# Performance work log

Measured on AMD Instinct MI355X. Metric: run time of the kernel, lower is better.

## Reference

```python
import jax, jax.numpy as jnp
import numpy as np

B, S, D = 4, 1024, 2048
NH, NKV, HD = 16, 8, 128
N_EXP, TOP_K, RANK, ALPHA = 4, 2, 16, 32
LORA_SCALE = ALPHA / RANK
EPS = 1e-6
NEG_INF = -1e9


def setup_inputs() -> dict:
    key = jax.random.key(0)
    ks = jax.random.split(key, 12)
    inv_freq = 1.0 / (10000.0 ** (jnp.arange(0, HD, 2, dtype=jnp.float32) / HD))
    pos = jnp.arange(S, dtype=jnp.float32)
    freqs = pos[:, None] * inv_freq[None, :]            # [S, HD/2]
    emb = jnp.concatenate([freqs, freqs], axis=-1)      # [S, HD]
    cos = jnp.broadcast_to(jnp.cos(emb)[None], (B, S, HD))
    sin = jnp.broadcast_to(jnp.sin(emb)[None], (B, S, HD))
    s = 0.02
    return {
        "hidden_states": jax.random.normal(ks[0], (B, S, D), jnp.float32),
        "cos": cos,
        "sin": sin,
        "Wq": jax.random.normal(ks[1], (NH * HD, D), jnp.float32) * s,
        "Wk": jax.random.normal(ks[2], (NKV * HD, D), jnp.float32) * s,
        "Wv": jax.random.normal(ks[3], (NKV * HD, D), jnp.float32) * s,
        "Wo": jax.random.normal(ks[4], (D, NH * HD), jnp.float32) * s,
        "q_norm_w": jnp.ones((HD,), jnp.float32),
        "k_norm_w": jnp.ones((HD,), jnp.float32),
        "gate_w": jax.random.normal(ks[5], (N_EXP, D), jnp.float32) * s,
        "loraA": jax.random.normal(ks[6], (N_EXP, RANK, NH * HD), jnp.float32) * s,
        "loraB": jax.random.normal(ks[7], (N_EXP, D, RANK), jnp.float32) * s,
    }


def _rms_norm(x, w):
    # per-head-dim RMSNorm (Qwen3 style), computed in fp32
    var = jnp.mean(jnp.square(x.astype(jnp.float32)), axis=-1, keepdims=True)
    return (x.astype(jnp.float32) * jax.lax.rsqrt(var + EPS)).astype(x.dtype) * w


def _rotate_half(x):
    x1, x2 = jnp.split(x, 2, axis=-1)
    return jnp.concatenate([-x2, x1], axis=-1)


def reference(hidden_states, cos, sin, Wq, Wk, Wv, Wo, q_norm_w, k_norm_w, gate_w, loraA, loraB):
    b, s, d = hidden_states.shape
    scaling = HD ** -0.5

    # ---- router (top-k of softmax over 4 experts) ----
    flat = hidden_states.reshape(-1, d)                       # [T, D]
    router_logits = flat @ gate_w.T                           # [T, E]
    probs = jax.nn.softmax(router_logits.astype(jnp.float32), axis=-1)
    top_w, top_idx = jax.lax.top_k(probs, TOP_K)              # [T, K]
    top_w = top_w.astype(hidden_states.dtype)
    # dense per-expert weight: [T, E]
    expert_w = jnp.sum(jax.nn.one_hot(top_idx, N_EXP, dtype=top_w.dtype) * top_w[..., None], axis=1)

    # ---- QKV projections + per-head RMSNorm ----
    q = (hidden_states @ Wq.T).reshape(b, s, NH, HD)
    k = (hidden_states @ Wk.T).reshape(b, s, NKV, HD)
    v = (hidden_states @ Wv.T).reshape(b, s, NKV, HD)
    q = _rms_norm(q, q_norm_w).transpose(0, 2, 1, 3)          # [B, NH, S, HD]
    k = _rms_norm(k, k_norm_w).transpose(0, 2, 1, 3)          # [B, NKV, S, HD]
    v = v.transpose(0, 2, 1, 3)

    # ---- RoPE ----
    c, sn = cos[:, None], sin[:, None]                        # [B, 1, S, HD]
    q = q * c + _rotate_half(q) * sn
    k = k * c + _rotate_half(k) * sn

    # ---- GQA repeat + eager attention ----
    n_rep = NH // NKV
    k = jnp.repeat(k, n_rep, axis=1)
    v = jnp.repeat(v, n_rep, axis=1)
    attn = jnp.einsum('bhqd,bhkd->bhqk', q, k) * scaling
    causal = jnp.tril(jnp.ones((s, s), bool))
    attn = jnp.where(causal[None, None], attn, NEG_INF)
    attn_w = jax.nn.softmax(attn.astype(jnp.float32), axis=-1).astype(q.dtype)
    attn_out = jnp.einsum('bhqk,bhkd->bqhd', attn_w, v).reshape(b, s, NH * HD)

    # ---- base output projection + LoRA expert mixture ----
    base = attn_out @ Wo.T                                    # [B, S, D]
    x = attn_out.reshape(-1, NH * HD)                         # [T, NH*HD]
    h = jnp.einsum('td,erd->ter', x, loraA)                   # [T, E, R]
    delta = jnp.einsum('ter,edr->ted', h, loraB) * LORA_SCALE # [T, E, D]
    expert_out = jnp.einsum('te,ted->td', expert_w, delta).reshape(b, s, d)

    return base + expert_out
```

## Files before the change

### kernel.cpp

```cpp
#include <hip/hip_runtime.h>
#include <hip/hip_bf16.h>

#define S_LEN   1024
#define BATCH   4
#define DMODEL  2048
#define NHEADS  16
#define NKVH    8
#define HEADD   128
#define NTOK    4096
#define QKV_CH  4096

typedef __bf16 bf16x8 __attribute__((ext_vector_type(8)));
typedef float  f32x4  __attribute__((ext_vector_type(4)));

__device__ __forceinline__ float bf2f(unsigned short u) {
    return __uint_as_float(((unsigned)u) << 16);
}
__device__ __forceinline__ ushort f2bu(float f) {
    union { __hip_bfloat16 h; ushort u; } c;
    c.h = __float2bfloat16(f);
    return c.u;
}
__device__ __forceinline__ void gl_lds16(const ushort* g, ushort* l) {
    __builtin_amdgcn_global_load_lds(
        (const __attribute__((address_space(1))) void*)g,
        (__attribute__((address_space(3))) void*)l,
        16, 0, 0);
}

__global__ __launch_bounds__(256) void prep_kernel(const float* __restrict__ Wq,
                                                   const float* __restrict__ Wk,
                                                   const float* __restrict__ Wv,
                                                   const float* __restrict__ Wo,
                                                   const float* __restrict__ lA,
                                                   const float* __restrict__ lB,
                                                   const float* __restrict__ cosb,
                                                   const float* __restrict__ sinb,
                                                   const float* __restrict__ X,
                                                   const float* __restrict__ GW,
                                                   __hip_bfloat16* __restrict__ wqkv,
                                                   __hip_bfloat16* __restrict__ wo,
                                                   __hip_bfloat16* __restrict__ acat,
                                                   __hip_bfloat16* __restrict__ Xb,
                                                   float* __restrict__ EW,
                                                   ushort* __restrict__ Bt,
                                                   float4* __restrict__ cs4) {
    __shared__ float red[4][257];
    const int blk = blockIdx.x, tid = threadIdx.x;

    if (blk < 12416) {
        int i = blk * 256 + tid;
        const float* src; __hip_bfloat16* dst; int off;
        if (i < 1048576)      { src = Wq; dst = wqkv;           off = i; }
        else if (i < 1572864) { src = Wk; dst = wqkv + 4194304; off = i - 1048576; }
        else if (i < 2097152) { src = Wv; dst = wqkv + 6291456; off = i - 1572864; }
        else if (i < 3145728) { src = Wo; dst = wo;             off = i - 2097152; }
        else if (i < 3178496) { src = lA; dst = acat;           off = i - 3145728; }
        else return;
        float4 v = ((const float4*)src)[off];
        union { ushort4 u; __hip_bfloat16 h[4]; } r;
        r.h[0] = __float2bfloat16(v.x);
        r.h[1] = __float2bfloat16(v.y);
        r.h[2] = __float2bfloat16(v.z);
        r.h[3] = __float2bfloat16(v.w);
        ((ushort4*)dst)[off] = r.u;
    } else if (blk < 16512) {
        const int t = blk - 12416;
        const float* x = X + (size_t)t * DMODEL;
        __hip_bfloat16* xb = Xb + (size_t)t * DMODEL;
        float p0 = 0.f, p1 = 0.f, p2 = 0.f, p3 = 0.f;
#pragma unroll
        for (int c = 0; c < 2; c++) {
            int i4 = tid + c * 256;
            float4 v = ((const float4*)x)[i4];
            union { ushort4 u; __hip_bfloat16 h[4]; } r;
            r.h[0] = __float2bfloat16(v.x);
            r.h[1] = __float2bfloat16(v.y);
            r.h[2] = __float2bfloat16(v.z);
            r.h[3] = __float2bfloat16(v.w);
            ((ushort4*)xb)[i4] = r.u;
            int d = i4 * 4;
            const float* g0 = GW + d;
            p0 += v.x * g0[0] + v.y * g0[1] + v.z * g0[2] + v.w * g0[3];
            const float* g1 = GW + DMODEL + d;
            p1 += v.x * g1[0] + v.y * g1[1] + v.z * g1[2] + v.w * g1[3];
            const float* g2 = GW + 2 * DMODEL + d;
            p2 += v.x * g2[0] + v.y * g2[1] + v.z * g2[2] + v.w * g2[3];
            const float* g3 = GW + 3 * DMODEL + d;
            p3 += v.x * g3[0] + v.y * g3[1] + v.z * g3[2] + v.w * g3[3];
        }
        red[0][tid] = p0; red[1][tid] = p1; red[2][tid] = p2; red[3][tid] = p3;
        __syncthreads();
        for (int s = 128; s > 0; s >>= 1) {
            if (tid < s) {
                red[0][tid] += red[0][tid + s];
                red[1][tid] += red[1][tid + s];
                red[2][tid] += red[2][tid + s];
                red[3][tid] += red[3][tid + s];
            }
            __syncthreads();
        }
        if (tid == 0) {
            float l[4] = { red[0][0], red[1][0], red[2][0], red[3][0] };
            float mx = fmaxf(fmaxf(l[0], l[1]), fmaxf(l[2], l[3]));
            float pe[4], sum = 0.f;
            for (int e = 0; e < 4; e++) { pe[e] = __expf(l[e] - mx); sum += pe[e]; }
            float inv = 1.0f / sum;
            for (int e = 0; e < 4; e++) pe[e] *= inv;
            int i1 = 0;
            for (int e = 1; e < 4; e++) if (pe[e] > pe[i1]) i1 = e;
            int i2 = -1;
            for (int e = 0; e < 4; e++) if (e != i1 && (i2 < 0 || pe[e] > pe[i2])) i2 = e;
            float o[4] = {0.f, 0.f, 0.f, 0.f};
            o[i1] = pe[i1]; o[i2] = pe[i2];
            float* ew = EW + (size_t)t * 4;
            ew[0] = o[0]; ew[1] = o[1]; ew[2] = o[2]; ew[3] = o[3];
        }
    } else {
        const int bblk = blk - 16512;
        if (bblk < 512) {
            int idx = bblk * 256 + tid;
            int d = idx >> 6, er = idx & 63;
            int e = er >> 4, r = er & 15;
            Bt[idx] = f2bu(lB[((size_t)e * DMODEL + d) * 16 + r]);
        } else {
            int idx = (bblk - 512) * 256 + tid;
            int s = idx >> 6, d0 = idx & 63;
            const float* cp = cosb + (size_t)s * HEADD;
            const float* sp = sinb + (size_t)s * HEADD;
            cs4[idx] = make_float4(cp[d0], cp[d0 + 64], sp[d0], sp[d0 + 64]);
        }
    }
}

#define LDSA0 0
#define LDSB0 16384
#define LDSA1 32768
#define LDSB1 49152

#define FENCE_BAR() do { asm volatile("" ::: "memory"); __builtin_amdgcn_s_barrier(); } while (0)

__device__ __forceinline__ void stage_half(const ushort* src, ushort* dst, size_t ld) {
    gl_lds16(src, dst);
    gl_lds16(src + (size_t)64 * ld, dst + 4096);
}

#define PHASE_MFMA_PRE()  do { \
    asm volatile("" ::: "memory"); \
    __builtin_amdgcn_s_barrier(); \
    asm volatile("s_waitcnt lgkmcnt(0)" ::: "memory"); \
    __builtin_amdgcn_sched_barrier(0); \
    __builtin_amdgcn_s_setprio(1); } while (0)

#define PHASE_MFMA_POST() do { \
    __builtin_amdgcn_s_setprio(0); } while (0)

__device__ __forceinline__ void ktile(const ushort* As, const ushort* Bs,
                                      f32x4 (&acc)[8][4],
                                      int aBase, int bBase, int cs0, int cs1,
                                      const ushort* s1s, ushort* s1d, bool s12en,
                                      const ushort* s2s, ushort* s2d,
                                      const ushort* s3s, ushort* s3d, bool s34en,
                                      const ushort* s4s, ushort* s4d,
                                      int K, bool lastVm)
{
    bf16x8 a0[4][2], a1[4][2], b0[2][2], b1[2][2];

#pragma unroll
    for (int ii = 0; ii < 4; ii++) {
        a0[ii][0] = *(const bf16x8*)(As + aBase + ii * 2048 + cs0);
        a0[ii][1] = *(const bf16x8*)(As + aBase + ii * 2048 + cs1);
    }
#pragma unroll
    for (int jj = 0; jj < 2; jj++) {
        b0[jj][0] = *(const bf16x8*)(Bs + bBase + jj * 4096 + cs0);
        b0[jj][1] = *(const bf16x8*)(Bs + bBase + jj * 4096 + cs1);
    }
    if (s12en) stage_half(s1s, s1d, K);
    asm volatile("s_waitcnt lgkmcnt(8)" ::: "memory");
    PHASE_MFMA_PRE();
#pragma unroll
    for (int k = 0; k < 2; k++)
#pragma unroll
        for (int ii = 0; ii < 4; ii++)
#pragma unroll
            for (int jj = 0; jj < 2; jj++)
                acc[ii][2 * jj] = __builtin_amdgcn_mfma_f32_16x16x32_bf16(
                    a0[ii][k], b0[jj][k], acc[ii][2 * jj], 0, 0, 0);
    PHASE_MFMA_POST();
    FENCE_BAR();

#pragma unroll
    for (int jj = 0; jj < 2; jj++) {
        b1[jj][0] = *(const bf16x8*)(Bs + bBase + 8192 + jj * 4096 + cs0);
        b1[jj][1] = *(const bf16x8*)(Bs + bBase + 8192 + jj * 4096 + cs1);
    }
    if (s12en) stage_half(s2s, s2d, K);
    PHASE_MFMA_PRE();
#pragma unroll
    for (int k = 0; k < 2; k++)
#pragma unroll
        for (int ii = 0; ii < 4; ii++)
#pragma unroll
            for (int jj = 0; jj < 2; jj++)
                acc[ii][1 + 2 * jj] = __builtin_amdgcn_mfma_f32_16x16x32_bf16(
                    a0[ii][k], b1[jj][k], acc[ii][1 + 2 * jj], 0, 0, 0);
    PHASE_MFMA_POST();
    FENCE_BAR();

#pragma unroll
    for (int ii = 0; ii < 4; ii++) {
        a1[ii][0] = *(const bf16x8*)(As + aBase + 8192 + ii * 2048 + cs0);
        a1[ii][1] = *(const bf16x8*)(As + aBase + 8192 + ii * 2048 + cs1);
    }
    if (s34en) stage_half(s3s, s3d, K);
    PHASE_MFMA_PRE();
#pragma unroll
    for (int k = 0; k < 2; k++)
#pragma unroll
        for (int ii = 0; ii < 4; ii++)
#pragma unroll
            for (int jj = 0; jj < 2; jj++)
                acc[4 + ii][2 * jj] = __builtin_amdgcn_mfma_f32_16x16x32_bf16(
                    a1[ii][k], b0[jj][k], acc[4 + ii][2 * jj], 0, 0, 0);
    PHASE_MFMA_POST();
    FENCE_BAR();

    if (s34en) stage_half(s4s, s4d, K);
    asm volatile("" ::: "memory");
    __builtin_amdgcn_s_barrier();
    __builtin_amdgcn_sched_barrier(0);
    __builtin_amdgcn_s_setprio(1);
#pragma unroll
    for (int k = 0; k < 2; k++)
#pragma unroll
        for (int ii = 0; ii < 4; ii++)
#pragma unroll
            for (int jj = 0; jj < 2; jj++)
                acc[4 + ii][1 + 2 * jj] = __builtin_amdgcn_mfma_f32_16x16x32_bf16(
                    a1[ii][k], b1[jj][k], acc[4 + ii][1 + 2 * jj], 0, 0, 0);
    __builtin_amdgcn_s_setprio(0);
    if (lastVm) { asm volatile("s_waitcnt vmcnt(0)" ::: "memory"); }
    else        { asm volatile("s_waitcnt vmcnt(4)" ::: "memory"); }
    __builtin_amdgcn_s_barrier();
}

__global__ __launch_bounds__(512, 2) void gemm256(const ushort* __restrict__ A,
                                                  const ushort* __restrict__ B,
                                                  const float4* __restrict__ cs4,
                                                  const float* __restrict__ qnw,
                                                  const float* __restrict__ knw,
                                                  ushort* __restrict__ Qb,
                                                  ushort* __restrict__ Kb,
                                                  ushort* __restrict__ Vt,
                                                  int K) {
    __shared__ __align__(16) ushort lds[65536];
    const int tid  = threadIdx.x;
    const int wave = tid >> 6, lane = tid & 63;
    const int l16  = lane & 15, quad = lane >> 4;
    const int wm = wave >> 2, wn = wave & 3;

    const int wg0 = blockIdx.x;
    const int swz = (wg0 & 7) * 32 + (wg0 >> 3);
    const int m0 = (swz >> 4) * 256, n0 = (swz & 15) * 256;

    const int srow = tid >> 3;
    const int scol = ((tid & 7) * 8) ^ ((srow & 7) << 3);
    const ushort* aSrc = A + (size_t)(m0 + srow) * K + scol;
    const ushort* bSrc = B + (size_t)(n0 + srow) * K + scol;

    const int aBase = (wm * 16 + l16) * 64;
    const int bBase = (wn * 16 + l16) * 64;
    const int cs0 = ((0 + quad) ^ (l16 & 7)) * 8;
    const int cs1 = ((4 + quad) ^ (l16 & 7)) * 8;

    f32x4 acc[8][4];
#pragma unroll
    for (int i = 0; i < 8; i++)
#pragma unroll
        for (int j = 0; j < 4; j++) acc[i][j] = (f32x4){0.f, 0.f, 0.f, 0.f};

    const int NT = K >> 6;

    const ushort* A0s = lds + LDSA0;
    const ushort* B0s = lds + LDSB0;
    const ushort* A1s = lds + LDSA1;
    const ushort* B1s = lds + LDSB1;

    stage_half(aSrc,                     lds + LDSA0 + tid * 8, K);
    stage_half(aSrc + (size_t)128 * K,   lds + LDSA0 + 8192 + tid * 8, K);
    stage_half(bSrc,                     lds + LDSB0 + tid * 8, K);
    stage_half(bSrc + (size_t)128 * K,   lds + LDSB0 + 8192 + tid * 8, K);
    stage_half(aSrc + 64,                lds + LDSA1 + tid * 8, K);
    stage_half(bSrc + 64,                lds + LDSB1 + tid * 8, K);
    asm volatile("s_waitcnt vmcnt(4)" ::: "memory");
    __builtin_amdgcn_s_barrier();

    for (int t = 0; t + 1 < NT; t += 2) {
        const bool s34 = (t + 2) < NT, s78 = (t + 3) < NT;
        const int k1 = (t + 1) * 64, k2 = (t + 2) * 64, k3 = (t + 3) * 64;

        ktile(A0s, B0s, acc, aBase, bBase, cs0, cs1,
              aSrc + (size_t)128 * K + k1, lds + LDSA1 + 8192 + tid * 8, true,
              bSrc + (size_t)128 * K + k1, lds + LDSB1 + 8192 + tid * 8,
              aSrc + k2,                   lds + LDSA0 + tid * 8, s34,
              bSrc + k2,                   lds + LDSB0 + tid * 8,
              K, !s34);

        ktile(A1s, B1s, acc, aBase, bBase, cs0, cs1,
              aSrc + (size_t)128 * K + k2, lds + LDSA0 + 8192 + tid * 8, s34,
              bSrc + (size_t)128 * K + k2, lds + LDSB0 + 8192 + tid * 8,
              aSrc + k3,                   lds + LDSA1 + tid * 8, s78,
              bSrc + k3,                   lds + LDSB1 + tid * 8,
              K, !s78);
    }

    const int nb = n0 >> 8;
    if (nb < 12) {
        const bool isQ = (nb < 8);
        const float scale = isQ ? 0.08838834764831845f : 1.0f;
        const float* nw = isQ ? qnw : knw;
        const int d0 = wn * 16 + l16;
        const float w0 = nw[d0] * scale, w1 = nw[d0 + 64] * scale;
        const int h0 = isQ ? (n0 >> 7) : ((n0 - 2048) >> 7);
        const int nh = isQ ? 16 : 8;
        ushort* gbase = isQ ? Qb : Kb;
        float* fsq = (float*)(lds + 32768);
        const float4* cvrow = cs4 + ((m0 & 1023) * 64 + d0);

#pragma unroll
        for (int half = 0; half < 2; half++) {
#pragma unroll
            for (int i2 = 0; i2 < 4; i2++)
#pragma unroll
                for (int r = 0; r < 4; r++) {
                    const int i = half * 4 + i2;
                    const int r128 = i2 * 32 + wm * 16 + quad * 4 + r;
#pragma unroll
                    for (int h = 0; h < 2; h++) {
                        float x1 = acc[i][h][r], x2 = acc[i][h + 2][r];
                        float p = x1 * x1 + x2 * x2;
                        p += __shfl_xor(p, 1);
                        p += __shfl_xor(p, 2);
                        p += __shfl_xor(p, 4);
                        p += __shfl_xor(p, 8);
                        if (l16 == 0) fsq[(r128 * 2 + h) * 4 + wn] = p;
                    }
                }
            __syncthreads();

#pragma unroll
            for (int i2 = 0; i2 < 4; i2++)
#pragma unroll
                for (int r = 0; r < 4; r++) {
                    const int i = half * 4 + i2;
                    const int r128 = i2 * 32 + wm * 16 + quad * 4 + r;
                    const float4 cv = cvrow[(size_t)(half * 128 + r128) * 64];
                    const int sw = ((r128 >> 2) & 3) << 4;
                    ushort* lrow = lds + r128 * 256;
#pragma unroll
                    for (int h = 0; h < 2; h++) {
                        const float* q4 = fsq + (r128 * 2 + h) * 4;
                        float ssq = q4[0] + q4[1] + q4[2] + q4[3];
                        float rstd = rsqrtf(ssq * (1.0f / 128.0f) + 1e-6f);
                        float n1 = acc[i][h][r] * rstd * w0;
                        float n2 = acc[i][h + 2][r] * rstd * w1;
                        lrow[(h * 128 + d0) ^ sw]      = f2bu(n1 * cv.x - n2 * cv.z);
                        lrow[(h * 128 + d0 + 64) ^ sw] = f2bu(n2 * cv.y + n1 * cv.w);
                    }
                }
            __syncthreads();

#pragma unroll
            for (int g = 0; g < 8; g++) {
                int gg = tid + g * 512;
                int row = gg >> 5, colg = gg & 31;
                int col8 = colg * 8;
                int sw = ((row >> 2) & 3) << 4;
                uint4 v = *(const uint4*)(lds + row * 256 + (col8 ^ sw));
                int head = col8 >> 7, d = col8 & 127;
                int tok = m0 + half * 128 + row;
                int b = tok >> 10, s = tok & 1023;
                *(uint4*)(gbase + ((size_t)((b * nh + h0 + head) * 1024 + s)) * HEADD + d) = v;
            }
            __syncthreads();
        }
    } else {
#pragma unroll
        for (int i = 0; i < 8; i++)
#pragma unroll
            for (int j = 0; j < 4; j++) {
                int coll = (j & 1) * 128 + (j >> 1) * 64 + wn * 16 + l16;
                int xr = (coll & 7) << 3;
#pragma unroll
                for (int r = 0; r < 4; r++) {
                    int rowl = (i & 3) * 32 + (i >> 2) * 128 + wm * 16 + quad * 4 + r;
                    lds[coll * 256 + (rowl ^ xr)] = f2bu(acc[i][j][r]);
                }
            }
        __syncthreads();
        const int b = m0 >> 10, s0 = m0 & 1023;
        const int kv0 = (n0 - 3072) >> 7;
#pragma unroll
        for (int g = 0; g < 16; g++) {
            int gg = tid + g * 512;
            int d = gg >> 5, sg = gg & 31;
            uint4 v = *(const uint4*)(lds + d * 256 + ((sg * 8) ^ ((d & 7) << 3)));
            int kv = kv0 + (d >> 7), dh = d & 127;
            *(uint4*)(Vt + ((size_t)((b * 8 + kv) * 128 + dh)) * 1024 + s0 + sg * 8) = v;
        }
    }
}

#define WO_A0 0
#define WO_A1 16384
#define WO_B0 32768
#define WO_B1 40960

__device__ __forceinline__ void wo_tile(const ushort* As, const ushort* Bs,
                                        f32x4 (&acc)[8][2],
                                        int aBase, int bBase, int cs0, int cs1,
                                        const ushort* s1s, ushort* s1d, size_t s1ld, bool s1en,
                                        const ushort* s2as, ushort* s2ad,
                                        const ushort* s2bs, ushort* s2bd, size_t s2ld, bool s2en,
                                        bool lastVm)
{
    bf16x8 a0[4][2], a1[4][2], b[2][2];

#pragma unroll
    for (int ii = 0; ii < 4; ii++) {
        a0[ii][0] = *(const bf16x8*)(As + aBase + ii * 2048 + cs0);
        a0[ii][1] = *(const bf16x8*)(As + aBase + ii * 2048 + cs1);
    }
#pragma unroll
    for (int jj = 0; jj < 2; jj++) {
        b[jj][0] = *(const bf16x8*)(Bs + bBase + jj * 4096 + cs0);
        b[jj][1] = *(const bf16x8*)(Bs + bBase + jj * 4096 + cs1);
    }
    if (s1en) stage_half(s1s, s1d, s1ld);
    asm volatile("s_waitcnt lgkmcnt(8)" ::: "memory");
    PHASE_MFMA_PRE();
#pragma unroll
    for (int k = 0; k < 2; k++)
#pragma unroll
        for (int ii = 0; ii < 4; ii++)
#pragma unroll
            for (int jj = 0; jj < 2; jj++)
                acc[ii][jj] = __builtin_amdgcn_mfma_f32_16x16x32_bf16(
                    a0[ii][k], b[jj][k], acc[ii][jj], 0, 0, 0);
    PHASE_MFMA_POST();
    FENCE_BAR();

#pragma unroll
    for (int ii = 0; ii < 4; ii++) {
        a1[ii][0] = *(const bf16x8*)(As + aBase + 8192 + ii * 2048 + cs0);
        a1[ii][1] = *(const bf16x8*)(As + aBase + 8192 + ii * 2048 + cs1);
    }
    if (s2en) { stage_half(s2as, s2ad, s2ld); stage_half(s2bs, s2bd, s2ld); }
    PHASE_MFMA_PRE();
#pragma unroll
    for (int k = 0; k < 2; k++)
#pragma unroll
        for (int ii = 0; ii < 4; ii++)
#pragma unroll
            for (int jj = 0; jj < 2; jj++)
                acc[4 + ii][jj] = __builtin_amdgcn_mfma_f32_16x16x32_bf16(
                    a1[ii][k], b[jj][k], acc[4 + ii][jj], 0, 0, 0);
    PHASE_MFMA_POST();
    if (lastVm) { asm volatile("s_waitcnt vmcnt(0)" ::: "memory"); }
    else        { asm volatile("s_waitcnt vmcnt(4)" ::: "memory"); }
    __builtin_amdgcn_s_barrier();
}

__global__ __launch_bounds__(512, 2) void gemm_wo(const ushort* __restrict__ A,
                                                  const ushort* __restrict__ B,
                                                  const ushort* __restrict__ A2,
                                                  const ushort* __restrict__ B2,
                                                  float* __restrict__ C) {
    __shared__ __align__(16) ushort lds[49152];
    const int tid  = threadIdx.x;
    const int wave = tid >> 6, lane = tid & 63;
    const int l16  = lane & 15, quad = lane >> 4;
    const int wm = wave >> 2, wn = wave & 3;
    const int K = DMODEL, N = DMODEL;

    const int wg0 = blockIdx.x;
    const int swz = (wg0 & 7) * 32 + (wg0 >> 3);
    const int m0 = (swz >> 4) * 256, n0 = (swz & 15) * 128;

    const int srow = tid >> 3;
    const int scol = ((tid & 7) * 8) ^ ((srow & 7) << 3);
    const ushort* aSrc  = A  + (size_t)(m0 + srow) * K + scol;
    const ushort* bSrc  = B  + (size_t)(n0 + srow) * K + scol;
    const ushort* a2Src = A2 + (size_t)(m0 + srow) * 64 + scol;
    const ushort* b2Src = B2 + (size_t)(n0 + srow) * 64 + scol;

    const int aBase = (wm * 16 + l16) * 64;
    const int bBase = (wn * 16 + l16) * 64;
    const int cs0 = ((0 + quad) ^ (l16 & 7)) * 8;
    const int cs1 = ((4 + quad) ^ (l16 & 7)) * 8;

    f32x4 acc[8][2];
#pragma unroll
    for (int i = 0; i < 8; i++)
#pragma unroll
        for (int j = 0; j < 2; j++) acc[i][j] = (f32x4){0.f, 0.f, 0.f, 0.f};

    const ushort* A0s = lds + WO_A0;
    const ushort* B0s = lds + WO_B0;
    const ushort* A1s = lds + WO_A1;
    const ushort* B1s = lds + WO_B1;

    stage_half(aSrc,                   lds + WO_A0 + tid * 8, K);
    stage_half(aSrc + (size_t)128 * K, lds + WO_A0 + 8192 + tid * 8, K);
    stage_half(bSrc,                   lds + WO_B0 + tid * 8, K);
    stage_half(aSrc + 64,              lds + WO_A1 + tid * 8, K);
    stage_half(bSrc + 64,              lds + WO_B1 + tid * 8, K);
    asm volatile("s_waitcnt vmcnt(4)" ::: "memory");
    __builtin_amdgcn_s_barrier();

    for (int t = 0; t < 32; t += 2) {
        const int u1 = t + 1, u2 = t + 2, u3 = t + 3;
        const bool l2 = (u2 == 32);
        const bool s3en = (u3 <= 32);

        const ushort* s2as = l2 ? a2Src : (aSrc + (size_t)u2 * 64);
        const ushort* s2bs = l2 ? b2Src : (bSrc + (size_t)u2 * 64);
        const size_t  s2ld = l2 ? (size_t)64 : (size_t)K;
        wo_tile(A0s, B0s, acc, aBase, bBase, cs0, cs1,
                aSrc + (size_t)128 * K + (size_t)u1 * 64, lds + WO_A1 + 8192 + tid * 8, K, true,
                s2as, lds + WO_A0 + tid * 8,
                s2bs, lds + WO_B0 + tid * 8, s2ld, true,
                false);

        const ushort* s1s = l2 ? (a2Src + (size_t)128 * 64)
                               : (aSrc + (size_t)128 * K + (size_t)u2 * 64);
        const size_t  s1ld = l2 ? (size_t)64 : (size_t)K;
        wo_tile(A1s, B1s, acc, aBase, bBase, cs0, cs1,
                s1s, lds + WO_A0 + 8192 + tid * 8, s1ld, true,
                aSrc + (size_t)u3 * 64, lds + WO_A1 + tid * 8,
                bSrc + (size_t)u3 * 64, lds + WO_B1 + tid * 8, K, s3en,
                !s3en);
    }
    wo_tile(A0s, B0s, acc, aBase, bBase, cs0, cs1,
            nullptr, nullptr, K, false,
            nullptr, nullptr, nullptr, nullptr, K, false,
            true);

    float* crow = C + (size_t)(m0 + wm * 16 + quad * 4) * N + n0 + wn * 16 + l16;
#pragma unroll
    for (int i = 0; i < 8; i++) {
        float* cpi = crow + (size_t)((i & 3) * 32 + (i >> 2) * 128) * N;
#pragma unroll
        for (int r = 0; r < 4; r++)
#pragma unroll
            for (int jj = 0; jj < 2; jj++)
                cpi[(size_t)r * N + jj * 64] = acc[i][jj][r];
    }
}

__global__ __launch_bounds__(256) void lora_h_kernel(const ushort* __restrict__ X,
                                                     const ushort* __restrict__ Acat,
                                                     const float* __restrict__ EW,
                                                     ushort* __restrict__ G) {
    __shared__ ushort As[64 * 64];
    __shared__ ushort Bs[64 * 64];
    const int tid = threadIdx.x;
    const int wave = tid >> 6, lane = tid & 63;
    const int l16 = lane & 15, quad = lane >> 4;
    const int m0 = blockIdx.x * 64;

    f32x4 acc[4];
#pragma unroll
    for (int nt = 0; nt < 4; nt++) acc[nt] = (f32x4){0.f, 0.f, 0.f, 0.f};

    const int r1 = tid >> 3;
    const int scol = ((tid & 7) * 8) ^ ((r1 & 7) << 3);
    const int cs0 = ((0 + quad) ^ (l16 & 7)) * 8;
    const int cs1 = ((4 + quad) ^ (l16 & 7)) * 8;

    for (int k0 = 0; k0 < DMODEL; k0 += 64) {
        __syncthreads();
        gl_lds16(X + (size_t)(m0 + r1) * DMODEL + k0 + scol, As + tid * 8);
        gl_lds16(X + (size_t)(m0 + 32 + r1) * DMODEL + k0 + scol, As + 2048 + tid * 8);
        gl_lds16(Acat + (size_t)r1 * DMODEL + k0 + scol, Bs + tid * 8);
        gl_lds16(Acat + (size_t)(32 + r1) * DMODEL + k0 + scol, Bs + 2048 + tid * 8);
        __syncthreads();
        bf16x8 af0 = *(const bf16x8*)(As + (wave * 16 + l16) * 64 + cs0);
        bf16x8 af1 = *(const bf16x8*)(As + (wave * 16 + l16) * 64 + cs1);
#pragma unroll
        for (int nt = 0; nt < 4; nt++) {
            bf16x8 b0 = *(const bf16x8*)(Bs + (nt * 16 + l16) * 64 + cs0);
            acc[nt] = __builtin_amdgcn_mfma_f32_16x16x32_bf16(af0, b0, acc[nt], 0, 0, 0);
            bf16x8 b1 = *(const bf16x8*)(Bs + (nt * 16 + l16) * 64 + cs1);
            acc[nt] = __builtin_amdgcn_mfma_f32_16x16x32_bf16(af1, b1, acc[nt], 0, 0, 0);
        }
    }
#pragma unroll
    for (int nt = 0; nt < 4; nt++)
#pragma unroll
        for (int r = 0; r < 4; r++) {
            int m = m0 + wave * 16 + quad * 4 + r;
            float wsc = 2.0f * EW[(size_t)m * 4 + nt];
            G[(size_t)m * 64 + nt * 16 + l16] = f2bu(acc[nt][r] * wsc);
        }
}

#define VPITCH 72
__global__ __launch_bounds__(256) void fattn_kernel(const ushort* __restrict__ Qb,
                                                    const ushort* __restrict__ Kb,
                                                    const ushort* __restrict__ Vt,
                                                    __hip_bfloat16* __restrict__ O) {
    __shared__ __align__(16) ushort Ks[2][64 * 128];
    __shared__ __align__(16) ushort Vs[2][128 * 64];
    __shared__ __align__(16) ushort Ps[4 * 16 * VPITCH];
    const int tid = threadIdx.x;
    const int wq = tid >> 6, lane = tid & 63;
    const int l16 = lane & 15, quad = lane >> 4;
    const int qblk = 15 - (blockIdx.x >> 6);
    const int bh = blockIdx.x & 63;
    const int b = bh >> 4, h = bh & 15;
    const int kvb = b * 8 + (h >> 1);
    const int q0 = qblk * 64;
    const int qbase = q0 + wq * 16;

    bf16x8 qf[4];
    const ushort* qrow = Qb + ((size_t)bh * S_LEN + qbase + l16) * HEADD;
#pragma unroll
    for (int kt = 0; kt < 4; kt++)
        qf[kt] = *(const bf16x8*)(qrow + kt * 32 + quad * 8);

    f32x4 oacc[8];
#pragma unroll
    for (int dt = 0; dt < 8; dt++) oacc[dt] = (f32x4){0.f, 0.f, 0.f, 0.f};
    float l[4] = { 0.f, 0.f, 0.f, 0.f };

    const ushort* kbase = Kb + (size_t)kvb * S_LEN * HEADD;
    const ushort* vbase = Vt + (size_t)kvb * HEADD * S_LEN;
    const int ntiles = qblk + 1;

    const int kr = tid >> 4, kc = ((tid & 15) * 8) ^ ((( tid >> 4) & 7) << 3);
    const int vr = tid >> 3, vc = ((tid & 7) * 8) ^ ((( tid >> 3) & 7) << 3);
    const int xrK = (l16 & 7) << 3;

#pragma unroll
    for (int c = 0; c < 4; c++) {
        gl_lds16(kbase + (size_t)(c * 16 + kr) * HEADD + kc, &Ks[0][c * 2048 + tid * 8]);
        gl_lds16(vbase + (size_t)(c * 32 + vr) * S_LEN + vc, &Vs[0][c * 2048 + tid * 8]);
    }

    for (int kb = 0; kb < ntiles; kb++) {
        const int cur = kb & 1;
        const int k0 = kb * 64;
        if (kb + 1 < ntiles) {
            const int k0n = k0 + 64;
#pragma unroll
            for (int c = 0; c < 4; c++) {
                gl_lds16(kbase + (size_t)(k0n + c * 16 + kr) * HEADD + kc,
                         &Ks[cur ^ 1][c * 2048 + tid * 8]);
                gl_lds16(vbase + (size_t)(c * 32 + vr) * S_LEN + k0n + vc,
                         &Vs[cur ^ 1][c * 2048 + tid * 8]);
            }
            asm volatile("s_waitcnt vmcnt(8)" ::: "memory");
        } else {
            asm volatile("s_waitcnt vmcnt(0)" ::: "memory");
        }
        __builtin_amdgcn_s_barrier();
        const ushort* Kc = Ks[cur];
        const ushort* Vc = Vs[cur];

        f32x4 sacc[4];
#pragma unroll
        for (int nt = 0; nt < 4; nt++) sacc[nt] = (f32x4){0.f, 0.f, 0.f, 0.f};
        __builtin_amdgcn_s_setprio(1);
#pragma unroll
        for (int kt = 0; kt < 4; kt++) {
#pragma unroll
            for (int nt = 0; nt < 4; nt++) {
                bf16x8 kf = *(const bf16x8*)(Kc + (nt * 16 + l16) * 128 + ((kt * 32 + quad * 8) ^ xrK));
                sacc[nt] = __builtin_amdgcn_mfma_f32_16x16x32_bf16(qf[kt], kf, sacc[nt], 0, 0, 0);
            }
        }
        __builtin_amdgcn_s_setprio(0);

#pragma unroll
        for (int r = 0; r < 4; r++) {
            const int qg = qbase + quad * 4 + r;
#pragma unroll
            for (int nt = 0; nt < 4; nt++) {
                int kg = k0 + nt * 16 + l16;
                float p = (kg <= qg) ? __expf(sacc[nt][r]) : 0.f;
                l[r] += p;
                Ps[wq * 16 * VPITCH + (quad * 4 + r) * VPITCH + nt * 16 + l16] = f2bu(p);
            }
        }

        __builtin_amdgcn_s_setprio(1);
#pragma unroll
        for (int kt2 = 0; kt2 < 2; kt2++) {
            bf16x8 pf = *(const bf16x8*)(Ps + wq * 16 * VPITCH + l16 * VPITCH + kt2 * 32 + quad * 8);
#pragma unroll
            for (int dt = 0; dt < 8; dt++) {
                bf16x8 vf = *(const bf16x8*)(Vc + (dt * 16 + l16) * 64 + ((kt2 * 32 + quad * 8) ^ xrK));
                oacc[dt] = __builtin_amdgcn_mfma_f32_16x16x32_bf16(pf, vf, oacc[dt], 0, 0, 0);
            }
        }
        __builtin_amdgcn_s_setprio(0);
        asm volatile("" ::: "memory");
        __builtin_amdgcn_s_barrier();
    }

#pragma unroll
    for (int r = 0; r < 4; r++) {
        float lr = l[r];
        lr += __shfl_xor(lr, 1);
        lr += __shfl_xor(lr, 2);
        lr += __shfl_xor(lr, 4);
        lr += __shfl_xor(lr, 8);
        float inv = 1.0f / lr;
        size_t base = ((size_t)(b * S_LEN + qbase + quad * 4 + r)) * (NHEADS * HEADD) + h * HEADD;
#pragma unroll
        for (int dt = 0; dt < 8; dt++)
            O[base + dt * 16 + l16] = __float2bfloat16(oacc[dt][r] * inv);
    }
}

extern "C" void kernel_launch(void* const* d_in, const int* in_sizes, int n_in,
                              void* d_out, int out_size, void* d_ws, size_t ws_size,
                              hipStream_t stream) {
    const float* hidden = (const float*)d_in[0];
    const float* cosb   = (const float*)d_in[1];
    const float* sinb   = (const float*)d_in[2];
    const float* Wq     = (const float*)d_in[3];
    const float* Wk     = (const float*)d_in[4];
    const float* Wv     = (const float*)d_in[5];
    const float* Wo     = (const float*)d_in[6];
    const float* qnw    = (const float*)d_in[7];
    const float* knw    = (const float*)d_in[8];
    const float* gw     = (const float*)d_in[9];
    const float* lA     = (const float*)d_in[10];
    const float* lB     = (const float*)d_in[11];
    float* out = (float*)d_out;

    char* ws = (char*)d_ws;
    __hip_bfloat16* hid_bf  = (__hip_bfloat16*)ws;
    __hip_bfloat16* wqkv_bf = (__hip_bfloat16*)(ws + (16u << 20));
    __hip_bfloat16* wo_bf   = (__hip_bfloat16*)(ws + (32u << 20));
    ushort*         Qb      = (ushort*)(ws + (40u << 20));
    ushort*         Kb      = (ushort*)(ws + (56u << 20));
    ushort*         Vt      = (ushort*)(ws + (64u << 20));
    __hip_bfloat16* attn_bf = (__hip_bfloat16*)(ws + (72u << 20));
    ushort*         Acat    = (ushort*)(ws + (104u << 20));
    ushort*         Bt      = (ushort*)(ws + (104u << 20) + (256u << 10));
    ushort*         G       = (ushort*)(ws + (104u << 20) + (512u << 10));
    float*          ew      = (float*)(ws + (105u << 20));
    float4*         cs4     = (float4*)(ws + (106u << 20));

    prep_kernel<<<17280, 256, 0, stream>>>(Wq, Wk, Wv, Wo, lA, lB, cosb, sinb,
                                           hidden, gw,
                                           wqkv_bf, wo_bf, (__hip_bfloat16*)Acat,
                                           hid_bf, ew, Bt, cs4);

    gemm256<<<256, 512, 0, stream>>>((const ushort*)hid_bf, (const ushort*)wqkv_bf,
                                     cs4, qnw, knw, Qb, Kb, Vt, DMODEL);

    fattn_kernel<<<1024, 256, 0, stream>>>(Qb, Kb, Vt, attn_bf);

    lora_h_kernel<<<64, 256, 0, stream>>>((const ushort*)attn_bf, Acat, ew, G);

    gemm_wo<<<256, 512, 0, stream>>>((const ushort*)attn_bf, (const ushort*)wo_bf,
                                     G, Bt, out);
}
```

Before: 313.3 us.

## Process two adjacent query blocks per attention workgroup to share K/V tiles

Each flash-attention workgroup now handles a pair of adjacent 64-row query blocks. Every K/V tile is loaded into LDS once and used by both blocks, and the lower block skips tiles beyond its causal limit. The grid shrinks from 1024 to 512 blocks, with heavier pairs scheduled first. This cuts global K/V traffic and barrier count per query row. In exchange it doubles the accumulator register footprint, which may reduce occupancy, and it leaves fewer, more unevenly sized blocks.

After: 322.6 us. 3.0% more time.

```diff
diff --git a/kernel.cpp b/kernel.cpp
--- a/kernel.cpp
+++ b/kernel.cpp
@@ -607,6 +607,51 @@
 }
 
 #define VPITCH 72
+__device__ __forceinline__ void attn_tile(const ushort* Kc, const ushort* Vc,
+                                          ushort* PsW,
+                                          const bf16x8 (&qf)[4], f32x4 (&oacc)[8],
+                                          float (&lsum)[4],
+                                          int qbase, int k0, int l16, int quad, int xrK)
+{
+    f32x4 sacc[4];
+#pragma unroll
+    for (int nt = 0; nt < 4; nt++) sacc[nt] = (f32x4){0.f, 0.f, 0.f, 0.f};
+    __builtin_amdgcn_s_setprio(1);
+#pragma unroll
+    for (int kt = 0; kt < 4; kt++) {
+#pragma unroll
+        for (int nt = 0; nt < 4; nt++) {
+            bf16x8 kf = *(const bf16x8*)(Kc + (nt * 16 + l16) * 128 + ((kt * 32 + quad * 8) ^ xrK));
+            sacc[nt] = __builtin_amdgcn_mfma_f32_16x16x32_bf16(qf[kt], kf, sacc[nt], 0, 0, 0);
+        }
+    }
+    __builtin_amdgcn_s_setprio(0);
+
+#pragma unroll
+    for (int r = 0; r < 4; r++) {
+        const int qg = qbase + quad * 4 + r;
+#pragma unroll
+        for (int nt = 0; nt < 4; nt++) {
+            int kg = k0 + nt * 16 + l16;
+            float p = (kg <= qg) ? __expf(sacc[nt][r]) : 0.f;
+            lsum[r] += p;
+            PsW[(quad * 4 + r) * VPITCH + nt * 16 + l16] = f2bu(p);
+        }
+    }
+
+    __builtin_amdgcn_s_setprio(1);
+#pragma unroll
+    for (int kt2 = 0; kt2 < 2; kt2++) {
+        bf16x8 pf = *(const bf16x8*)(PsW + l16 * VPITCH + kt2 * 32 + quad * 8);
+#pragma unroll
+        for (int dt = 0; dt < 8; dt++) {
+            bf16x8 vf = *(const bf16x8*)(Vc + (dt * 16 + l16) * 64 + ((kt2 * 32 + quad * 8) ^ xrK));
+            oacc[dt] = __builtin_amdgcn_mfma_f32_16x16x32_bf16(pf, vf, oacc[dt], 0, 0, 0);
+        }
+    }
+    __builtin_amdgcn_s_setprio(0);
+}
+
 __global__ __launch_bounds__(256) void fattn_kernel(const ushort* __restrict__ Qb,
                                                     const ushort* __restrict__ Kb,
                                                     const ushort* __restrict__ Vt,
@@ -617,31 +662,40 @@
     const int tid = threadIdx.x;
     const int wq = tid >> 6, lane = tid & 63;
     const int l16 = lane & 15, quad = lane >> 4;
-    const int qblk = 15 - (blockIdx.x >> 6);
+    const int qpair = (blockIdx.x < 256) ? (7 - (blockIdx.x >> 6)) : ((blockIdx.x >> 6) - 4);
     const int bh = blockIdx.x & 63;
     const int b = bh >> 4, h = bh & 15;
     const int kvb = b * 8 + (h >> 1);
-    const int q0 = qblk * 64;
-    const int qbase = q0 + wq * 16;
-
-    bf16x8 qf[4];
-    const ushort* qrow = Qb + ((size_t)bh * S_LEN + qbase + l16) * HEADD;
-#pragma unroll
-    for (int kt = 0; kt < 4; kt++)
-        qf[kt] = *(const bf16x8*)(qrow + kt * 32 + quad * 8);
-
-    f32x4 oacc[8];
-#pragma unroll
-    for (int dt = 0; dt < 8; dt++) oacc[dt] = (f32x4){0.f, 0.f, 0.f, 0.f};
-    float l[4] = { 0.f, 0.f, 0.f, 0.f };
+    const int qblkA = qpair * 2, qblkB = qpair * 2 + 1;
+    const int qbaseA = qblkA * 64 + wq * 16;
+    const int qbaseB = qblkB * 64 + wq * 16;
+
+    bf16x8 qfA[4], qfB[4];
+    const ushort* qrowA = Qb + ((size_t)bh * S_LEN + qbaseA + l16) * HEADD;
+    const ushort* qrowB = Qb + ((size_t)bh * S_LEN + qbaseB + l16) * HEADD;
+#pragma unroll
+    for (int kt = 0; kt < 4; kt++) {
+        qfA[kt] = *(const bf16x8*)(qrowA + kt * 32 + quad * 8);
+        qfB[kt] = *(const bf16x8*)(qrowB + kt * 32 + quad * 8);
+    }
+
+    f32x4 oaccA[8], oaccB[8];
+#pragma unroll
+    for (int dt = 0; dt < 8; dt++) {
+        oaccA[dt] = (f32x4){0.f, 0.f, 0.f, 0.f};
+        oaccB[dt] = (f32x4){0.f, 0.f, 0.f, 0.f};
+    }
+    float lsumA[4] = { 0.f, 0.f, 0.f, 0.f };
+    float lsumB[4] = { 0.f, 0.f, 0.f, 0.f };
 
     const ushort* kbase = Kb + (size_t)kvb * S_LEN * HEADD;
     const ushort* vbase = Vt + (size_t)kvb * HEADD * S_LEN;
-    const int ntiles = qblk + 1;
+    const int ntiles = qblkB + 1;
 
     const int kr = tid >> 4, kc = ((tid & 15) * 8) ^ ((( tid >> 4) & 7) << 3);
     const int vr = tid >> 3, vc = ((tid & 7) * 8) ^ ((( tid >> 3) & 7) << 3);
     const int xrK = (l16 & 7) << 3;
+    ushort* PsW = Ps + wq * 16 * VPITCH;
 
 #pragma unroll
     for (int c = 0; c < 4; c++) {
@@ -669,59 +723,37 @@
         const ushort* Kc = Ks[cur];
         const ushort* Vc = Vs[cur];
 
-        f32x4 sacc[4];
-#pragma unroll
-        for (int nt = 0; nt < 4; nt++) sacc[nt] = (f32x4){0.f, 0.f, 0.f, 0.f};
-        __builtin_amdgcn_s_setprio(1);
-#pragma unroll
-        for (int kt = 0; kt < 4; kt++) {
-#pragma unroll
-            for (int nt = 0; nt < 4; nt++) {
-                bf16x8 kf = *(const bf16x8*)(Kc + (nt * 16 + l16) * 128 + ((kt * 32 + quad * 8) ^ xrK));
-                sacc[nt] = __builtin_amdgcn_mfma_f32_16x16x32_bf16(qf[kt], kf, sacc[nt], 0, 0, 0);
-            }
-        }
-        __builtin_amdgcn_s_setprio(0);
-
-#pragma unroll
-        for (int r = 0; r < 4; r++) {
-            const int qg = qbase + quad * 4 + r;
-#pragma unroll
-            for (int nt = 0; nt < 4; nt++) {
-                int kg = k0 + nt * 16 + l16;
-                float p = (kg <= qg) ? __expf(sacc[nt][r]) : 0.f;
-                l[r] += p;
-                Ps[wq * 16 * VPITCH + (quad * 4 + r) * VPITCH + nt * 16 + l16] = f2bu(p);
-            }
-        }
-
-        __builtin_amdgcn_s_setprio(1);
-#pragma unroll
-        for (int kt2 = 0; kt2 < 2; kt2++) {
-            bf16x8 pf = *(const bf16x8*)(Ps + wq * 16 * VPITCH + l16 * VPITCH + kt2 * 32 + quad * 8);
-#pragma unroll
-            for (int dt = 0; dt < 8; dt++) {
-                bf16x8 vf = *(const bf16x8*)(Vc + (dt * 16 + l16) * 64 + ((kt2 * 32 + quad * 8) ^ xrK));
-                oacc[dt] = __builtin_amdgcn_mfma_f32_16x16x32_bf16(pf, vf, oacc[dt], 0, 0, 0);
-            }
-        }
-        __builtin_amdgcn_s_setprio(0);
+        attn_tile(Kc, Vc, PsW, qfB, oaccB, lsumB, qbaseB, k0, l16, quad, xrK);
+        if (kb <= qblkA)
+            attn_tile(Kc, Vc, PsW, qfA, oaccA, lsumA, qbaseA, k0, l16, quad, xrK);
+
         asm volatile("" ::: "memory");
         __builtin_amdgcn_s_barrier();
     }
 
 #pragma unroll
     for (int r = 0; r < 4; r++) {
-        float lr = l[r];
-        lr += __shfl_xor(lr, 1);
-        lr += __shfl_xor(lr, 2);
-        lr += __shfl_xor(lr, 4);
-        lr += __shfl_xor(lr, 8);
-        float inv = 1.0f / lr;
-        size_t base = ((size_t)(b * S_LEN + qbase + quad * 4 + r)) * (NHEADS * HEADD) + h * HEADD;
+        float lrA = lsumA[r];
+        lrA += __shfl_xor(lrA, 1);
+        lrA += __shfl_xor(lrA, 2);
+        lrA += __shfl_xor(lrA, 4);
+        lrA += __shfl_xor(lrA, 8);
+        float invA = 1.0f / lrA;
+        size_t baseA = ((size_t)(b * S_LEN + qbaseA + quad * 4 + r)) * (NHEADS * HEADD) + h * HEADD;
 #pragma unroll
         for (int dt = 0; dt < 8; dt++)
-            O[base + dt * 16 + l16] = __float2bfloat16(oacc[dt][r] * inv);
+            O[baseA + dt * 16 + l16] = __float2bfloat16(oaccA[dt][r] * invA);
+
+        float lrB = lsumB[r];
+        lrB += __shfl_xor(lrB, 1);
+        lrB += __shfl_xor(lrB, 2);
+        lrB += __shfl_xor(lrB, 4);
+        lrB += __shfl_xor(lrB, 8);
+        float invB = 1.0f / lrB;
+        size_t baseB = ((size_t)(b * S_LEN + qbaseB + quad * 4 + r)) * (NHEADS * HEADD) + h * HEADD;
+#pragma unroll
+        for (int dt = 0; dt < 8; dt++)
+            O[baseB + dt * 16 + l16] = __float2bfloat16(oaccB[dt][r] * invB);
     }
 }
 
@@ -764,7 +796,7 @@
     gemm256<<<256, 512, 0, stream>>>((const ushort*)hid_bf, (const ushort*)wqkv_bf,
                                      cs4, qnw, knw, Qb, Kb, Vt, DMODEL);
 
-    fattn_kernel<<<1024, 256, 0, stream>>>(Qb, Kb, Vt, attn_bf);
+    fattn_kernel<<<512, 256, 0, stream>>>(Qb, Kb, Vt, attn_bf);
 
     lora_h_kernel<<<64, 256, 0, stream>>>((const ushort*)attn_bf, Acat, ew, G);
 
```
